# Performance work log

Hardware: AMD Instinct MI355X
Metric: run time of the kernel (lower is better)

## Reference

```python
import jax, jax.numpy as jnp
import numpy as np

HEADS = 8

def setup_inputs() -> dict:
    key = jax.random.key(0)
    ks = jax.random.split(key, 6)
    b, c, h, w = 32, 64, 56, 56
    m, dim = 6, 192
    inner = HEADS * c  # 512
    return {
        "x": jax.random.normal(ks[0], (b, c, h, w), dtype=jnp.float32),
        "z": jax.random.normal(ks[1], (b, m, dim), dtype=jnp.float32),
        "Wq": jax.random.normal(ks[2], (inner, dim), dtype=jnp.float32) * 0.05,
        "bq": jax.random.normal(ks[3], (inner,), dtype=jnp.float32) * 0.05,
        "Wo": jax.random.normal(ks[4], (dim, inner), dtype=jnp.float32) * 0.05,
        "bo": jax.random.normal(ks[5], (dim,), dtype=jnp.float32) * 0.05,
    }

def reference(x, z, Wq, bq, Wo, bo):
    b, c, h, w = x.shape
    _, m, d = z.shape
    heads = HEADS
    scale = d ** (-0.5)
    # torch: x.view(b, h*w, c) on contiguous (b,c,h,w) == plain reshape (memory reinterpretation)
    xf = x.reshape(b, h * w, c)
    # torch: repeat(1,1,heads) then view(b, heads, h*w, c) -- exact reshape semantics
    kv = jnp.tile(xf, (1, 1, heads)).reshape(b, heads, h * w, c)  # K = V
    # torch Linear: z @ Wq.T + bq, then view(b, heads, m, c)
    q = (jnp.einsum('bmd,id->bmi', z, Wq) + bq).reshape(b, heads, m, c)
    dots = jnp.einsum('bhmc,bhlc->bhml', q, kv) * scale
    attn = jax.nn.softmax(dots, axis=-1)
    out = jnp.einsum('bhml,bhlc->bhmc', attn, kv)
    out = out.transpose(0, 2, 1, 3).reshape(b, m, heads * c)  # 'b h m c -> b m (h c)'
    return z + jnp.einsum('bmi,di->bmd', out, Wo) + bo
```

## Files before the change

### kernel.cpp

```cpp
#include <hip/hip_runtime.h>
#include <math.h>

#define BATCH 32
#define NHEADS 8
#define M 6
#define DIM 192
#define CDIM 64
#define INNER 512
#define LFULL 3136
#define RDIST 392
#define EPITCH 400
#define NT2 1024
#define NGR 16

__global__ __launch_bounds__(NT2) void attn_kernel(const float* __restrict__ x,
                                                   const float* __restrict__ z,
                                                   const float* __restrict__ Wq,
                                                   const float* __restrict__ bq,
                                                   float* __restrict__ out2) {
    __shared__ float sQ[M * CDIM];
    __shared__ float sE[M][EPITCH];
    __shared__ float sPart[NGR][M * CDIM];
    __shared__ float sInv[M];

    const int b   = blockIdx.x / NHEADS;
    const int hh  = blockIdx.x % NHEADS;
    const int tid = threadIdx.x;

    if (tid < M * CDIM) {
        int gi = hh * (M * CDIM) + tid;
        int mz = gi / INNER;
        int iz = gi % INNER;
        const float4* zr = (const float4*)(z + (size_t)(b * M + mz) * DIM);
        const float4* wr = (const float4*)(Wq + (size_t)iz * DIM);
        float acc = bq[iz];
        #pragma unroll
        for (int j = 0; j < DIM / 4; ++j) {
            float4 a = zr[j], w = wr[j];
            acc += a.x * w.x + a.y * w.y + a.z * w.z + a.w * w.w;
        }
        sQ[tid] = acc * rsqrtf((float)DIM);
    }
    __syncthreads();

    const float* K = x + (size_t)b * (LFULL * CDIM) + (size_t)hh * (RDIST * CDIM);

    if (tid < 2 * RDIST) {
        int r  = tid >> 1;
        int mh = (tid & 1) * 3;
        const float4* kr = (const float4*)(K + (size_t)r * CDIM);
        const float4* q0 = (const float4*)(sQ + (mh    ) * CDIM);
        const float4* q1 = (const float4*)(sQ + (mh + 1) * CDIM);
        const float4* q2 = (const float4*)(sQ + (mh + 2) * CDIM);
        float d0 = 0.f, d1 = 0.f, d2 = 0.f;
        #pragma unroll
        for (int j = 0; j < CDIM / 4; ++j) {
            float4 k4 = kr[j];
            float4 a = q0[j];
            float4 bb = q1[j];
            float4 c = q2[j];
            d0 += k4.x * a.x  + k4.y * a.y  + k4.z * a.z  + k4.w * a.w;
            d1 += k4.x * bb.x + k4.y * bb.y + k4.z * bb.z + k4.w * bb.w;
            d2 += k4.x * c.x  + k4.y * c.y  + k4.z * c.z  + k4.w * c.w;
        }
        sE[mh    ][r] = __expf(d0);
        sE[mh + 1][r] = __expf(d1);
        sE[mh + 2][r] = __expf(d2);
    }
    __syncthreads();

    const int wave = tid >> 6;
    const int lane = tid & 63;

    if (wave < M) {
        float s = (lane < RDIST - 384) ? sE[wave][384 + lane] : 0.f;
        #pragma unroll
        for (int k = 0; k < 6; ++k) s += sE[wave][lane + 64 * k];
        #pragma unroll
        for (int off = 32; off; off >>= 1) s += __shfl_xor(s, off);
        if (lane == 0) sInv[wave] = 1.0f / s;
    }

    {
        float acc[M] = {0, 0, 0, 0, 0, 0};
        for (int r = wave; r < RDIST; r += NGR) {
            float kv = K[(size_t)r * CDIM + lane];
            #pragma unroll
            for (int mm = 0; mm < M; ++mm) acc[mm] += sE[mm][r] * kv;
        }
        #pragma unroll
        for (int mm = 0; mm < M; ++mm) sPart[wave][mm * CDIM + lane] = acc[mm];
    }
    __syncthreads();

    if (tid < M * CDIM) {
        float v = 0.f;
        #pragma unroll
        for (int g = 0; g < NGR; ++g) v += sPart[g][tid];
        int mm = tid >> 6, c = tid & 63;
        out2[(size_t)(b * M + mm) * INNER + hh * CDIM + c] = v * sInv[mm];
    }
}

__global__ __launch_bounds__(256) void oproj_kernel(const float* __restrict__ z,
                                                    const float* __restrict__ out2,
                                                    const float* __restrict__ Wo,
                                                    const float* __restrict__ bo,
                                                    float* __restrict__ out) {
    int g = blockIdx.x * blockDim.x + threadIdx.x;
    if (g >= BATCH * M * DIM) return;
    int dd = g % DIM;
    int bm = g / DIM;
    const float4* orow = (const float4*)(out2 + (size_t)bm * INNER);
    const float4* wrow = (const float4*)(Wo + (size_t)dd * INNER);
    float acc = bo[dd] + z[g];
    #pragma unroll 8
    for (int j = 0; j < INNER / 4; ++j) {
        float4 ov = orow[j];
        float4 wv = wrow[j];
        acc += ov.x * wv.x + ov.y * wv.y + ov.z * wv.z + ov.w * wv.w;
    }
    out[g] = acc;
}

extern "C" void kernel_launch(void* const* d_in, const int* in_sizes, int n_in,
                              void* d_out, int out_size, void* d_ws, size_t ws_size,
                              hipStream_t stream) {
    const float* x  = (const float*)d_in[0];
    const float* z  = (const float*)d_in[1];
    const float* Wq = (const float*)d_in[2];
    const float* bq = (const float*)d_in[3];
    const float* Wo = (const float*)d_in[4];
    const float* bo = (const float*)d_in[5];
    float* out = (float*)d_out;

    float* out2_ws = (float*)d_ws;

    attn_kernel<<<BATCH * NHEADS, NT2, 0, stream>>>(x, z, Wq, bq, out2_ws);
    oproj_kernel<<<(BATCH * M * DIM + 255) / 256, 256, 0, stream>>>(z, out2_ws, Wo, bo, out);
}
```

Measured before the change: 117.3 us.

## Split attention over key halves with atomic reductions and separate Q projection

```diff
diff --git a/kernel.cpp b/kernel.cpp
--- a/kernel.cpp
+++ b/kernel.cpp
@@ -9,43 +9,52 @@
 #define INNER 512
 #define LFULL 3136
 #define RDIST 392
-#define EPITCH 400
-#define NT2 1024
-#define NGR 16
+#define G 2
+#define RG 196
+#define EPITCH 200
+#define QN (BATCH * M * INNER)
 
-__global__ __launch_bounds__(NT2) void attn_kernel(const float* __restrict__ x,
-                                                   const float* __restrict__ z,
-                                                   const float* __restrict__ Wq,
-                                                   const float* __restrict__ bq,
-                                                   float* __restrict__ out2) {
+__global__ __launch_bounds__(256) void qproj_kernel(const float* __restrict__ z,
+                                                    const float* __restrict__ Wq,
+                                                    const float* __restrict__ bq,
+                                                    float* __restrict__ q) {
+    int g = blockIdx.x * blockDim.x + threadIdx.x;
+    if (g >= QN) return;
+    int iz = g % INNER;
+    int bm = g / INNER;
+    const float4* zrow = (const float4*)(z + (size_t)bm * DIM);
+    const float4* wrow = (const float4*)(Wq + (size_t)iz * DIM);
+    float acc = bq[iz];
+    #pragma unroll
+    for (int j = 0; j < DIM / 4; ++j) {
+        float4 zv = zrow[j], wv = wrow[j];
+        acc += zv.x * wv.x + zv.y * wv.y + zv.z * wv.z + zv.w * wv.w;
+    }
+    q[g] = acc;
+}
+
+__global__ __launch_bounds__(512) void attn_kernel(const float* __restrict__ x,
+                                                   const float* __restrict__ q,
+                                                   float* __restrict__ out2,
+                                                   float* __restrict__ S) {
     __shared__ float sQ[M * CDIM];
     __shared__ float sE[M][EPITCH];
-    __shared__ float sPart[NGR][M * CDIM];
-    __shared__ float sInv[M];
+    __shared__ float sPart[8][M * CDIM];
 
-    const int b   = blockIdx.x / NHEADS;
-    const int hh  = blockIdx.x % NHEADS;
+    const int blk = blockIdx.x;
+    const int gg  = blk & (G - 1);
+    const int hh  = (blk >> 1) & (NHEADS - 1);
+    const int b   = blk >> 4;
     const int tid = threadIdx.x;
 
-    if (tid < M * CDIM) {
-        int gi = hh * (M * CDIM) + tid;
-        int mz = gi / INNER;
-        int iz = gi % INNER;
-        const float4* zr = (const float4*)(z + (size_t)(b * M + mz) * DIM);
-        const float4* wr = (const float4*)(Wq + (size_t)iz * DIM);
-        float acc = bq[iz];
-        #pragma unroll
-        for (int j = 0; j < DIM / 4; ++j) {
-            float4 a = zr[j], w = wr[j];
-            acc += a.x * w.x + a.y * w.y + a.z * w.z + a.w * w.w;
-        }
-        sQ[tid] = acc * rsqrtf((float)DIM);
-    }
+    if (tid < M * CDIM) sQ[tid] = q[(size_t)b * (M * INNER) + hh * (M * CDIM) + tid];
     __syncthreads();
 
-    const float* K = x + (size_t)b * (LFULL * CDIM) + (size_t)hh * (RDIST * CDIM);
+    const float* K = x + (size_t)b * (LFULL * CDIM) + (size_t)hh * (RDIST * CDIM)
+                       + (size_t)gg * (RG * CDIM);
+    const float scale = rsqrtf((float)DIM);
 
-    if (tid < 2 * RDIST) {
+    if (tid < 2 * RG) {
         int r  = tid >> 1;
         int mh = (tid & 1) * 3;
         const float4* kr = (const float4*)(K + (size_t)r * CDIM);
@@ -56,16 +65,14 @@
         #pragma unroll
         for (int j = 0; j < CDIM / 4; ++j) {
             float4 k4 = kr[j];
-            float4 a = q0[j];
-            float4 bb = q1[j];
-            float4 c = q2[j];
+            float4 a = q0[j], bb = q1[j], c = q2[j];
             d0 += k4.x * a.x  + k4.y * a.y  + k4.z * a.z  + k4.w * a.w;
             d1 += k4.x * bb.x + k4.y * bb.y + k4.z * bb.z + k4.w * bb.w;
             d2 += k4.x * c.x  + k4.y * c.y  + k4.z * c.z  + k4.w * c.w;
         }
-        sE[mh    ][r] = __expf(d0);
-        sE[mh + 1][r] = __expf(d1);
-        sE[mh + 2][r] = __expf(d2);
+        sE[mh    ][r] = __expf(d0 * scale);
+        sE[mh + 1][r] = __expf(d1 * scale);
+        sE[mh + 2][r] = __expf(d2 * scale);
     }
     __syncthreads();
 
@@ -73,17 +80,16 @@
     const int lane = tid & 63;
 
     if (wave < M) {
-        float s = (lane < RDIST - 384) ? sE[wave][384 + lane] : 0.f;
-        #pragma unroll
-        for (int k = 0; k < 6; ++k) s += sE[wave][lane + 64 * k];
+        float s = sE[wave][lane] + sE[wave][lane + 64] + sE[wave][lane + 128];
+        if (lane < RG - 192) s += sE[wave][lane + 192];
         #pragma unroll
         for (int off = 32; off; off >>= 1) s += __shfl_xor(s, off);
-        if (lane == 0) sInv[wave] = 1.0f / s;
+        if (lane == 0) atomicAdd(S + ((b * NHEADS + hh) * M + wave), s);
     }
 
     {
         float acc[M] = {0, 0, 0, 0, 0, 0};
-        for (int r = wave; r < RDIST; r += NGR) {
+        for (int r = wave; r < RG; r += 8) {
             float kv = K[(size_t)r * CDIM + lane];
             #pragma unroll
             for (int mm = 0; mm < M; ++mm) acc[mm] += sE[mm][r] * kv;
@@ -96,14 +102,15 @@
     if (tid < M * CDIM) {
         float v = 0.f;
         #pragma unroll
-        for (int g = 0; g < NGR; ++g) v += sPart[g][tid];
+        for (int w = 0; w < 8; ++w) v += sPart[w][tid];
         int mm = tid >> 6, c = tid & 63;
-        out2[(size_t)(b * M + mm) * INNER + hh * CDIM + c] = v * sInv[mm];
+        atomicAdd(out2 + ((size_t)(b * M + mm) * INNER + hh * CDIM + c), v);
     }
 }
 
 __global__ __launch_bounds__(256) void oproj_kernel(const float* __restrict__ z,
                                                     const float* __restrict__ out2,
+                                                    const float* __restrict__ S,
                                                     const float* __restrict__ Wo,
                                                     const float* __restrict__ bo,
                                                     float* __restrict__ out) {
@@ -111,14 +118,19 @@
     if (g >= BATCH * M * DIM) return;
     int dd = g % DIM;
     int bm = g / DIM;
+    int b  = bm / M, mm = bm % M;
+
+    float inv[NHEADS];
+    #pragma unroll
+    for (int h = 0; h < NHEADS; ++h) inv[h] = 1.0f / S[(b * NHEADS + h) * M + mm];
+
     const float4* orow = (const float4*)(out2 + (size_t)bm * INNER);
     const float4* wrow = (const float4*)(Wo + (size_t)dd * INNER);
     float acc = bo[dd] + z[g];
     #pragma unroll 8
     for (int j = 0; j < INNER / 4; ++j) {
-        float4 ov = orow[j];
-        float4 wv = wrow[j];
-        acc += ov.x * wv.x + ov.y * wv.y + ov.z * wv.z + ov.w * wv.w;
+        float4 ov = orow[j], wv = wrow[j];
+        acc += (ov.x * wv.x + ov.y * wv.y + ov.z * wv.z + ov.w * wv.w) * inv[j >> 4];
     }
     out[g] = acc;
 }
@@ -134,8 +146,13 @@
     const float* bo = (const float*)d_in[5];
     float* out = (float*)d_out;
 
-    float* out2_ws = (float*)d_ws;
+    float* q_ws    = (float*)d_ws;
+    float* out2_ws = q_ws + QN;
+    float* S_ws    = out2_ws + QN;
 
-    attn_kernel<<<BATCH * NHEADS, NT2, 0, stream>>>(x, z, Wq, bq, out2_ws);
-    oproj_kernel<<<(BATCH * M * DIM + 255) / 256, 256, 0, stream>>>(z, out2_ws, Wo, bo, out);
+    hipMemsetAsync(out2_ws, 0, (QN + BATCH * NHEADS * M) * sizeof(float), stream);
+
+    qproj_kernel<<<(QN + 255) / 256, 256, 0, stream>>>(z, Wq, bq, q_ws);
+    attn_kernel<<<BATCH * NHEADS * G, 512, 0, stream>>>(x, q_ws, out2_ws, S_ws);
+    oproj_kernel<<<(BATCH * M * DIM + 255) / 256, 256, 0, stream>>>(z, out2_ws, S_ws, Wo, bo, out);
 }
```

Result: slower. 130.8 us (+11.5%).
